# Performance work log

Measured on AMD Instinct MI355X. Metric: run time of the kernel, lower is better.

Reference implementation:

```python
import jax, jax.numpy as jnp
import numpy as np

N = 100000      # nodes
F_IN = 500      # num_features
H = 128         # num_hidden
C = 40          # num_classes
E = 3200000     # structural edges
K = 5           # knn neighbors


def setup_inputs() -> dict:
    key = jax.random.key(0)
    ks = jax.random.split(key, 9)
    x = jax.random.normal(ks[0], (N, F_IN), dtype=jnp.float32)
    edge_index = jax.random.randint(ks[1], (2, E), 0, N, dtype=jnp.int64)
    # knn graph: source i repeated K times, targets random (stand-in for cosine-KNN)
    src = jnp.repeat(jnp.arange(N, dtype=jnp.int64), K)
    dst = jax.random.randint(ks[2], (K * N,), 0, N, dtype=jnp.int64)
    edge_index_knn = jnp.stack([src, dst])
    s = lambda f: np.float32(1.0 / np.sqrt(f))
    W1 = jax.random.normal(ks[3], (F_IN, H), jnp.float32) * s(F_IN)
    b1 = jnp.zeros((H,), jnp.float32)
    W2 = jax.random.normal(ks[4], (2 * H, C), jnp.float32) * s(2 * H)
    b2 = jnp.zeros((C,), jnp.float32)
    Wlin = jax.random.normal(ks[5], (C, 2 * C), jnp.float32) * s(2 * C)  # torch Linear layout [out,in]
    blin = jnp.zeros((C,), jnp.float32)
    return {"x": x, "edge_index": edge_index, "edge_index_knn": edge_index_knn,
            "W1": W1, "b1": b1, "W2": W2, "b2": b2, "Wlin": Wlin, "blin": blin}


def gcn_conv(x, W, b, edge_index):
    # PyG GCNConv: add self-loops, symmetric normalization deg^-1/2 A deg^-1/2, x@W, scatter-add, +bias
    n = x.shape[0]
    loop = jnp.arange(n, dtype=edge_index.dtype)
    row = jnp.concatenate([edge_index[0], loop])  # sources (gathered)
    col = jnp.concatenate([edge_index[1], loop])  # targets (scattered)
    deg = jax.ops.segment_sum(jnp.ones_like(col, x.dtype), col, num_segments=n)
    dinv = jnp.where(deg > 0, jax.lax.rsqrt(jnp.maximum(deg, 1e-12)), 0.0).astype(x.dtype)
    norm = dinv[row] * dinv[col]                      # [E+n]
    h = x @ W                                          # [n, out]
    agg = jax.ops.segment_sum(h[row] * norm[:, None], col, num_segments=n)
    return agg + b


def reference(x, edge_index, edge_index_knn, W1, b1, W2, b2, Wlin, blin):
    h1 = gcn_conv(x, W1, b1, edge_index)
    h1_2 = gcn_conv(x, W1, b1, edge_index_knn)
    R1 = jax.nn.relu(jnp.concatenate([h1, h1_2], axis=1))  # dropout identity (eval mode)
    h2 = gcn_conv(R1, W2, b2, edge_index)
    h2_2 = gcn_conv(R1, W2, b2, edge_index_knn)
    R2 = jnp.concatenate([h2, h2_2], axis=1)
    logits = R2 @ Wlin.T + blin
    return jax.nn.log_softmax(logits, axis=1)
```

## Files before the change

kernel.cpp:

```cpp
#include <hip/hip_runtime.h>
#include <stdint.h>

#define NN   100000
#define FIN  500
#define HID  128
#define KP1  512
#define K2   256
#define CO   40
#define NBUCK 391
#define CAPB_S 9216
#define CAPB_K 1536

typedef __attribute__((ext_vector_type(8))) short short8;
typedef __attribute__((ext_vector_type(4))) float float4v;
typedef __attribute__((address_space(3))) unsigned int as3_u32;
typedef __attribute__((address_space(1))) unsigned int as1_u32;

__device__ __forceinline__ unsigned short f2bf(float f) {
  unsigned u = __float_as_uint(f);
  u = u + 0x7fffu + ((u >> 16) & 1u);
  return (unsigned short)(u >> 16);
}
__device__ __forceinline__ float bf2f(unsigned short s) {
  return __uint_as_float(((unsigned)s) << 16);
}
__device__ __forceinline__ void gl_lds16(const void* g, void* l) {
  __builtin_amdgcn_global_load_lds((const as1_u32*)g, (as3_u32*)l, 16, 0, 0);
}

__global__ __launch_bounds__(256) void k_bin(
    const int* __restrict__ ei, int nS, int nb1S, int* __restrict__ gcur_s, int* __restrict__ gbin_s,
    const int* __restrict__ eik, int nK, int* __restrict__ gcur_k, int* __restrict__ gbin_k) {
  __shared__ int cnt[NBUCK];
  __shared__ int base[NBUCK];
  const int b = blockIdx.x;
  const bool knn = (b >= nb1S);
  const int* src = knn ? eik      : ei;
  const int* tgt = knn ? eik + nK : ei + nS;
  const int n    = knn ? nK : nS;
  int* gcur      = knn ? gcur_k : gcur_s;
  int* gbin      = knn ? gbin_k : gbin_s;
  const int capb = knn ? CAPB_K : CAPB_S;
  const int ebase = (knn ? b - nb1S : b) * 4096;
  const int t = threadIdx.x;

  for (int i = t; i < NBUCK; i += 256) cnt[i] = 0;
  __syncthreads();
  int s[16], g[16];
#pragma unroll
  for (int i = 0; i < 16; ++i) {
    const int e = ebase + i * 256 + t;
    const bool v = e < n;
    s[i] = v ? src[e] : 0;
    g[i] = v ? tgt[e] : -1;
    if (v) atomicAdd(&cnt[g[i] >> 8], 1);
  }
  __syncthreads();
  for (int i = t; i < NBUCK; i += 256) {
    const int c = cnt[i];
    base[i] = c ? atomicAdd(&gcur[i], c) : 0;
    cnt[i] = 0;
  }
  __syncthreads();
#pragma unroll
  for (int i = 0; i < 16; ++i) {
    if (g[i] >= 0) {
      const int bkt = g[i] >> 8;
      const int pos = base[bkt] + atomicAdd(&cnt[bkt], 1);
      if (pos < capb) gbin[bkt * capb + pos] = (s[i] << 8) | (g[i] & 255);
    }
  }
}

__global__ __launch_bounds__(512) void k_bscan(const int* __restrict__ gcur_s, int* __restrict__ bscan_s,
                                               const int* __restrict__ gcur_k, int* __restrict__ bscan_k) {
  __shared__ int sd[512];
  const int* gcur = blockIdx.x ? gcur_k : gcur_s;
  int* bscan      = blockIdx.x ? bscan_k : bscan_s;
  const int t = threadIdx.x;
  const int v = (t < NBUCK) ? gcur[t] : 0;
  sd[t] = v;
  __syncthreads();
  for (int off = 1; off < 512; off <<= 1) {
    const int x = (t >= off) ? sd[t - off] : 0;
    __syncthreads(); sd[t] += x; __syncthreads();
  }
  if (t < NBUCK) bscan[t] = sd[t] - v;
}

__global__ __launch_bounds__(256) void k_csr(
    const int* __restrict__ gcur_s, const int* __restrict__ gbin_s, const int* __restrict__ bscan_s,
    int* __restrict__ rp_s, int* __restrict__ col_s, float* __restrict__ dinv_s,
    const int* __restrict__ gcur_k, const int* __restrict__ gbin_k, const int* __restrict__ bscan_k,
    int* __restrict__ rp_k, int* __restrict__ col_k, float* __restrict__ dinv_k) {
  __shared__ int cnt[256];
  __shared__ int base[256];
  const int b0 = blockIdx.x;
  const bool knn = (b0 >= NBUCK);
  const int b = knn ? b0 - NBUCK : b0;
  const int* gcur  = knn ? gcur_k  : gcur_s;
  const int* gbin  = knn ? gbin_k  : gbin_s;
  const int* bscan = knn ? bscan_k : bscan_s;
  int* rp    = knn ? rp_k   : rp_s;
  int* col   = knn ? col_k  : col_s;
  float* dinv = knn ? dinv_k : dinv_s;
  const int capb = knn ? CAPB_K : CAPB_S;
  const int t = threadIdx.x;
  int nB = gcur[b]; if (nB > capb) nB = capb;
  const int gb0 = b * capb;
  const int gbase = bscan[b];

  cnt[t] = 0;
  __syncthreads();
  for (int i = t; i < nB; i += 256) atomicAdd(&cnt[gbin[gb0 + i] & 255], 1);
  __syncthreads();
  const int myc = cnt[t];
  base[t] = myc;
  __syncthreads();
  for (int off = 1; off < 256; off <<= 1) {
    const int x = (t >= off) ? base[t - off] : 0;
    __syncthreads(); base[t] += x; __syncthreads();
  }
  const int excl = base[t] - myc;
  const int tg = b * 256 + t;
  if (tg < NN) { rp[tg] = gbase + excl; dinv[tg] = rsqrtf((float)(myc + 1)); }
  if (tg == NN) rp[NN] = gbase + excl;
  __syncthreads();
  base[t] = excl; cnt[t] = 0;
  __syncthreads();
  for (int i = t; i < nB; i += 256) {
    const int e = gbin[gb0 + i];
    const int tl = e & 255;
    const int pos = atomicAdd(&cnt[tl], 1);
    col[gbase + base[tl] + pos] = e >> 8;
  }
}

__global__ void k_w1t(const float* __restrict__ W1, unsigned short* __restrict__ W1T) {
  int idx = blockIdx.x * 256 + threadIdx.x;
  int n = idx >> 9, k = idx & 511;
  float v = (k < FIN) ? W1[k * HID + n] : 0.f;
  W1T[idx] = f2bf(v);
}
__global__ void k_w2t(const float* __restrict__ W2, unsigned short* __restrict__ W2T) {
  int idx = blockIdx.x * 256 + threadIdx.x;
  int n = idx >> 8, k = idx & 255;
  float v = (n < CO) ? W2[k * CO + n] : 0.f;
  W2T[idx] = f2bf(v);
}

__global__ __launch_bounds__(256) void k_gemm1(const float* __restrict__ x,
    const unsigned short* __restrict__ W1T, const float* __restrict__ zbuf,
    unsigned short* __restrict__ H1b) {
  __shared__ float Als[1024 * 4];
  __shared__ unsigned short Bls[512 * 8];
  const int t = threadIdx.x;
  const int wv = t >> 6, lane = t & 63;
  const int qd = lane >> 4, mr = lane & 15;
  const int m0 = blockIdx.x * 128;

  float4v acc[2][8];
  const float4v zf4 = {0.f, 0.f, 0.f, 0.f};
#pragma unroll
  for (int a = 0; a < 2; ++a)
#pragma unroll
    for (int b = 0; b < 8; ++b) acc[a][b] = zf4;

  for (int kk = 0; kk < 16; ++kk) {
    const int k0 = kk * 32;
    __syncthreads();
#pragma unroll
    for (int i = 0; i < 4; ++i) {
      const int cb = (wv * 4 + i) * 64;
      const int q = cb + lane;
      const int kg = q >> 7, m = q & 127;
      const int gm = m0 + m, kb = k0 + kg * 4;
      const float* gp = (gm < NN && kb < FIN) ? (x + (size_t)gm * FIN + kb) : zbuf;
      gl_lds16(gp, &Als[cb * 4]);
    }
#pragma unroll
    for (int i = 0; i < 2; ++i) {
      const int cb = (wv * 2 + i) * 64;
      const int q = cb + lane;
      const int kg = q >> 7, n = q & 127;
      const unsigned short* gp = W1T + n * KP1 + k0 + kg * 8;
      gl_lds16(gp, &Bls[cb * 8]);
    }
    __syncthreads();
    short8 af[2];
#pragma unroll
    for (int rt = 0; rt < 2; ++rt) {
      const int m = wv * 32 + rt * 16 + mr;
      const float4v a0 = *(const float4v*)&Als[((2 * qd) * 128 + m) * 4];
      const float4v a1 = *(const float4v*)&Als[((2 * qd + 1) * 128 + m) * 4];
      short8 f;
      f[0] = (short)f2bf(a0[0]); f[1] = (short)f2bf(a0[1]);
      f[2] = (short)f2bf(a0[2]); f[3] = (short)f2bf(a0[3]);
      f[4] = (short)f2bf(a1[0]); f[5] = (short)f2bf(a1[1]);
      f[6] = (short)f2bf(a1[2]); f[7] = (short)f2bf(a1[3]);
      af[rt] = f;
    }
#pragma unroll
    for (int ct = 0; ct < 8; ++ct) {
      const short8 bf = *(const short8*)&Bls[(qd * 128 + ct * 16 + mr) * 8];
      acc[0][ct] = __builtin_amdgcn_mfma_f32_16x16x32_bf16(af[0], bf, acc[0][ct], 0, 0, 0);
      acc[1][ct] = __builtin_amdgcn_mfma_f32_16x16x32_bf16(af[1], bf, acc[1][ct], 0, 0, 0);
    }
  }
#pragma unroll
  for (int rt = 0; rt < 2; ++rt) {
    const int rb = m0 + wv * 32 + rt * 16 + qd * 4;
#pragma unroll
    for (int ct = 0; ct < 8; ++ct) {
      const int col = ct * 16 + mr;
#pragma unroll
      for (int j = 0; j < 4; ++j) {
        const int r = rb + j;
        if (r < NN) H1b[(size_t)r * HID + col] = f2bf(acc[rt][ct][j]);
      }
    }
  }
}

__global__ __launch_bounds__(256) void k_gemm2(const unsigned short* __restrict__ R1b,
    const unsigned short* __restrict__ W2T, const unsigned short* __restrict__ zbuf,
    unsigned short* __restrict__ H2b) {
  __shared__ unsigned short Als[512 * 8];
  __shared__ unsigned short Bls[192 * 8];
  const int t = threadIdx.x;
  const int wv = t >> 6, lane = t & 63;
  const int qd = lane >> 4, mr = lane & 15;
  const int m0 = blockIdx.x * 128;

  float4v acc[2][3];
  const float4v zf4 = {0.f, 0.f, 0.f, 0.f};
#pragma unroll
  for (int a = 0; a < 2; ++a)
#pragma unroll
    for (int b = 0; b < 3; ++b) acc[a][b] = zf4;

  for (int kk = 0; kk < 8; ++kk) {
    const int k0 = kk * 32;
    __syncthreads();
#pragma unroll
    for (int i = 0; i < 2; ++i) {
      const int cb = (wv * 2 + i) * 64;
      const int q = cb + lane;
      const int kg = q >> 7, m = q & 127;
      const int gm = m0 + m;
      const unsigned short* gp = (gm < NN) ? (R1b + (size_t)gm * K2 + k0 + kg * 8) : zbuf;
      gl_lds16(gp, &Als[cb * 8]);
    }
    if (wv < 3) {
      const int cb = wv * 64;
      const int q = cb + lane;
      const int kg = q / 48, n = q % 48;
      const unsigned short* gp = W2T + n * K2 + k0 + kg * 8;
      gl_lds16(gp, &Bls[cb * 8]);
    }
    __syncthreads();
    short8 af[2];
#pragma unroll
    for (int rt = 0; rt < 2; ++rt)
      af[rt] = *(const short8*)&Als[(qd * 128 + wv * 32 + rt * 16 + mr) * 8];
#pragma unroll
    for (int ct = 0; ct < 3; ++ct) {
      const short8 bf = *(const short8*)&Bls[(qd * 48 + ct * 16 + mr) * 8];
      acc[0][ct] = __builtin_amdgcn_mfma_f32_16x16x32_bf16(af[0], bf, acc[0][ct], 0, 0, 0);
      acc[1][ct] = __builtin_amdgcn_mfma_f32_16x16x32_bf16(af[1], bf, acc[1][ct], 0, 0, 0);
    }
  }
#pragma unroll
  for (int rt = 0; rt < 2; ++rt) {
    const int rb = m0 + wv * 32 + rt * 16 + qd * 4;
#pragma unroll
    for (int ct = 0; ct < 3; ++ct) {
      const int col = ct * 16 + mr;
      if (col < CO) {
#pragma unroll
        for (int j = 0; j < 4; ++j) {
          const int r = rb + j;
          if (r < NN) H2b[(size_t)r * CO + col] = f2bf(acc[rt][ct][j]);
        }
      }
    }
  }
}

__global__ __launch_bounds__(256) void k_agg1(
    const int* __restrict__ rp_s, const int* __restrict__ col_s, const float* __restrict__ dinv_s,
    const int* __restrict__ rp_k, const int* __restrict__ col_k, const float* __restrict__ dinv_k,
    const unsigned short* __restrict__ H, const float* __restrict__ bias,
    unsigned short* __restrict__ out, int nbS) {
  const int b = blockIdx.x;
  const bool knn = (b >= nbS);
  const int* rp = knn ? rp_k : rp_s;
  const int* ci = knn ? col_k : col_s;
  const float* dinv = knn ? dinv_k : dinv_s;
  const int colOff = knn ? HID : 0;
  const int wv = threadIdx.x >> 6, lane = threadIdx.x & 63;
  const int c = (knn ? b - nbS : b) * 4 + wv;
  if (c >= NN) return;
  const float dc = dinv[c];
  const unsigned pc = ((const unsigned*)(H + (size_t)c * HID))[lane];
  float ax = dc * bf2f((unsigned short)(pc & 0xffffu));
  float ay = dc * bf2f((unsigned short)(pc >> 16));
  int e = rp[c];
  const int e1 = rp[c + 1];
  for (; e + 4 <= e1; e += 4) {
    const int r0 = ci[e], r1 = ci[e + 1], r2 = ci[e + 2], r3 = ci[e + 3];
    const float d0 = dinv[r0], d1 = dinv[r1], d2 = dinv[r2], d3 = dinv[r3];
    const unsigned p0 = ((const unsigned*)(H + (size_t)r0 * HID))[lane];
    const unsigned p1 = ((const unsigned*)(H + (size_t)r1 * HID))[lane];
    const unsigned p2 = ((const unsigned*)(H + (size_t)r2 * HID))[lane];
    const unsigned p3 = ((const unsigned*)(H + (size_t)r3 * HID))[lane];
    ax += d0 * bf2f((unsigned short)(p0 & 0xffffu)) + d1 * bf2f((unsigned short)(p1 & 0xffffu))
        + d2 * bf2f((unsigned short)(p2 & 0xffffu)) + d3 * bf2f((unsigned short)(p3 & 0xffffu));
    ay += d0 * bf2f((unsigned short)(p0 >> 16)) + d1 * bf2f((unsigned short)(p1 >> 16))
        + d2 * bf2f((unsigned short)(p2 >> 16)) + d3 * bf2f((unsigned short)(p3 >> 16));
  }
  for (; e < e1; ++e) {
    const int r = ci[e];
    const float d = dinv[r];
    const unsigned pr = ((const unsigned*)(H + (size_t)r * HID))[lane];
    ax += d * bf2f((unsigned short)(pr & 0xffffu));
    ay += d * bf2f((unsigned short)(pr >> 16));
  }
  const float2 bb = ((const float2*)bias)[lane];
  const float o0 = fmaxf(dc * ax + bb.x, 0.f);
  const float o1 = fmaxf(dc * ay + bb.y, 0.f);
  const unsigned pk = (unsigned)f2bf(o0) | ((unsigned)f2bf(o1) << 16);
  ((unsigned*)(out + (size_t)c * (2 * HID) + colOff))[lane] = pk;
}

__global__ __launch_bounds__(256) void k_agg2(
    const int* __restrict__ rp_s, const int* __restrict__ col_s, const float* __restrict__ dinv_s,
    const int* __restrict__ rp_k, const int* __restrict__ col_k, const float* __restrict__ dinv_k,
    const unsigned short* __restrict__ H2, const float* __restrict__ bias,
    unsigned short* __restrict__ R2, int nbS) {
  const int b = blockIdx.x;
  const bool knn = (b >= nbS);
  const int* rp = knn ? rp_k : rp_s;
  const int* ci = knn ? col_k : col_s;
  const float* dinv = knn ? dinv_k : dinv_s;
  const int colOff = knn ? CO : 0;
  const int wv = threadIdx.x >> 6, lane = threadIdx.x & 63;
  const int c = (knn ? b - nbS : b) * 4 + wv;
  if (c >= NN || lane >= CO) return;
  const float dc = dinv[c];
  float acc = dc * bf2f(H2[(size_t)c * CO + lane]);
  int e = rp[c];
  const int e1 = rp[c + 1];
  for (; e + 4 <= e1; e += 4) {
    const int r0 = ci[e], r1 = ci[e + 1], r2 = ci[e + 2], r3 = ci[e + 3];
    const float d0 = dinv[r0], d1 = dinv[r1], d2 = dinv[r2], d3 = dinv[r3];
    acc += d0 * bf2f(H2[(size_t)r0 * CO + lane]) + d1 * bf2f(H2[(size_t)r1 * CO + lane])
         + d2 * bf2f(H2[(size_t)r2 * CO + lane]) + d3 * bf2f(H2[(size_t)r3 * CO + lane]);
  }
  for (; e < e1; ++e) {
    const int r = ci[e];
    acc += dinv[r] * bf2f(H2[(size_t)r * CO + lane]);
  }
  R2[(size_t)c * 80 + colOff + lane] = f2bf(dc * acc + bias[lane]);
}

__global__ __launch_bounds__(256) void k_final(const unsigned short* __restrict__ R2,
    const float* __restrict__ Wlin, const float* __restrict__ blin,
    float* __restrict__ out) {
  __shared__ float rw[32 * 81];
  __shared__ float wl[40 * 81];
  __shared__ float bl[40];
  const int t = threadIdx.x;
  const int n0 = blockIdx.x * 32;
  for (int i = t; i < 2560; i += 256) rw[(i / 80) * 81 + (i % 80)] = bf2f(R2[(size_t)n0 * 80 + i]);
  for (int i = t; i < 3200; i += 256) wl[(i / 80) * 81 + (i % 80)] = Wlin[i];
  if (t < 40) bl[t] = blin[t];
  __syncthreads();
  const int nl = t >> 3, jg = t & 7;
  const int j0 = jg * 5;
  float lg[5];
#pragma unroll
  for (int jj = 0; jj < 5; ++jj) lg[jj] = bl[j0 + jj];
#pragma unroll 4
  for (int k = 0; k < 80; ++k) {
    const float v = rw[nl * 81 + k];
#pragma unroll
    for (int jj = 0; jj < 5; ++jj) lg[jj] += v * wl[(j0 + jj) * 81 + k];
  }
  float mx = lg[0];
#pragma unroll
  for (int jj = 1; jj < 5; ++jj) mx = fmaxf(mx, lg[jj]);
  mx = fmaxf(mx, __shfl_xor(mx, 1));
  mx = fmaxf(mx, __shfl_xor(mx, 2));
  mx = fmaxf(mx, __shfl_xor(mx, 4));
  float s = 0.f;
#pragma unroll
  for (int jj = 0; jj < 5; ++jj) s += expf(lg[jj] - mx);
  s += __shfl_xor(s, 1);
  s += __shfl_xor(s, 2);
  s += __shfl_xor(s, 4);
  const float lse = mx + logf(s);
  const int n = n0 + nl;
#pragma unroll
  for (int jj = 0; jj < 5; ++jj) out[(size_t)n * CO + j0 + jj] = lg[jj] - lse;
}

extern "C" void kernel_launch(void* const* d_in, const int* in_sizes, int n_in,
                              void* d_out, int out_size, void* d_ws, size_t ws_size,
                              hipStream_t stream) {
  const float* x  = (const float*)d_in[0];
  const int* ei   = (const int*)d_in[1];
  const int* eik  = (const int*)d_in[2];
  const float* W1 = (const float*)d_in[3];
  const float* b1 = (const float*)d_in[4];
  const float* W2 = (const float*)d_in[5];
  const float* b2 = (const float*)d_in[6];
  const float* Wl = (const float*)d_in[7];
  const float* bl = (const float*)d_in[8];
  float* out = (float*)d_out;
  const int E  = in_sizes[1] / 2;
  const int EK = in_sizes[2] / 2;

  char* p = (char*)d_ws;
  size_t off = 0;
  auto alloc = [&](size_t bytes) -> void* {
    void* r = (void*)(p + off);
    off += (bytes + 255) & ~(size_t)255;
    return r;
  };
  int* gcur_s = (int*)alloc((size_t)NBUCK * 4);
  int* gcur_k = (int*)alloc((size_t)NBUCK * 4);
  void* zbuf = alloc(256);
  const size_t zero_span = off;
  int* bscan_s = (int*)alloc((size_t)NBUCK * 4);
  int* bscan_k = (int*)alloc((size_t)NBUCK * 4);
  float* dinv_s = (float*)alloc((size_t)NN * 4);
  float* dinv_k = (float*)alloc((size_t)NN * 4);
  int* rp_s = (int*)alloc((size_t)(NN + 1) * 4);
  int* rp_k = (int*)alloc((size_t)(NN + 1) * 4);
  unsigned short* W1T = (unsigned short*)alloc((size_t)HID * KP1 * 2);
  unsigned short* W2T = (unsigned short*)alloc((size_t)48 * K2 * 2);
  int* gbin_s = (int*)alloc((size_t)NBUCK * CAPB_S * 4);
  int* gbin_k = (int*)alloc((size_t)NBUCK * CAPB_K * 4);
  int* col_s = (int*)alloc((size_t)E * 4);
  int* col_k = (int*)alloc((size_t)EK * 4);
  unsigned short* H1b = (unsigned short*)alloc((size_t)NN * HID * 2);
  unsigned short* R1b = (unsigned short*)alloc((size_t)NN * K2 * 2);
  unsigned short* H2b = (unsigned short*)alloc((size_t)NN * CO * 2);
  unsigned short* R2  = H1b;

  hipMemsetAsync(d_ws, 0, zero_span, stream);

  const int nb1S = (E + 4095) / 4096;
  const int nb1K = (EK + 4095) / 4096;
  k_bin<<<nb1S + nb1K, 256, 0, stream>>>(ei, E, nb1S, gcur_s, gbin_s, eik, EK, gcur_k, gbin_k);
  k_bscan<<<2, 512, 0, stream>>>(gcur_s, bscan_s, gcur_k, bscan_k);
  k_csr<<<2 * NBUCK, 256, 0, stream>>>(gcur_s, gbin_s, bscan_s, rp_s, col_s, dinv_s,
                                       gcur_k, gbin_k, bscan_k, rp_k, col_k, dinv_k);

  k_w1t<<<(HID * KP1) / 256, 256, 0, stream>>>(W1, W1T);
  k_w2t<<<(48 * K2) / 256, 256, 0, stream>>>(W2, W2T);

  k_gemm1<<<(NN + 127) / 128, 256, 0, stream>>>(x, W1T, (const float*)zbuf, H1b);
  const int nbAgg = (NN + 3) / 4;
  k_agg1<<<2 * nbAgg, 256, 0, stream>>>(rp_s, col_s, dinv_s, rp_k, col_k, dinv_k,
                                        H1b, b1, R1b, nbAgg);

  k_gemm2<<<(NN + 127) / 128, 256, 0, stream>>>(R1b, W2T, (const unsigned short*)zbuf, H2b);
  k_agg2<<<2 * nbAgg, 256, 0, stream>>>(rp_s, col_s, dinv_s, rp_k, col_k, dinv_k,
                                        H2b, b2, R2, nbAgg);

  k_final<<<NN / 32, 256, 0, stream>>>(R2, Wl, bl, out);
}
```

Baseline: 793.8 us.

## Fold final linear into layer-2 weights, fuse aggregation with log-softmax, prebake edge weights

Layer 2 and the final linear are folded algebraically: W2 is premultiplied with the two halves of Wlin into an 80-column weight, and the biases into one constant vector. The second aggregation then reads the 80-wide P/Q product and applies log-softmax directly, which removes the H2/R2 round trips and the separate final kernel. A new pass stores each edge's source dinv next to its column index in an int2 CSR, so aggregation no longer does a dependent dinv gather. Layer-1 aggregation now handles both graphs per node in one wave and prefetches edges in batches of eight. The cost is doubled CSR index bytes, an extra fuse pass over all edges, and a change in where bf16 rounding happens.

```diff
diff --git a/kernel.cpp b/kernel.cpp
--- a/kernel.cpp
+++ b/kernel.cpp
@@ -7,6 +7,7 @@
 #define KP1  512
 #define K2   256
 #define CO   40
+#define NPQ  80
 #define NBUCK 391
 #define CAPB_S 9216
 #define CAPB_K 1536
@@ -90,9 +91,9 @@
 
 __global__ __launch_bounds__(256) void k_csr(
     const int* __restrict__ gcur_s, const int* __restrict__ gbin_s, const int* __restrict__ bscan_s,
-    int* __restrict__ rp_s, int* __restrict__ col_s, float* __restrict__ dinv_s,
+    int* __restrict__ rp_s, int2* __restrict__ colw_s, float* __restrict__ dinv_s,
     const int* __restrict__ gcur_k, const int* __restrict__ gbin_k, const int* __restrict__ bscan_k,
-    int* __restrict__ rp_k, int* __restrict__ col_k, float* __restrict__ dinv_k) {
+    int* __restrict__ rp_k, int2* __restrict__ colw_k, float* __restrict__ dinv_k) {
   __shared__ int cnt[256];
   __shared__ int base[256];
   const int b0 = blockIdx.x;
@@ -101,8 +102,8 @@
   const int* gcur  = knn ? gcur_k  : gcur_s;
   const int* gbin  = knn ? gbin_k  : gbin_s;
   const int* bscan = knn ? bscan_k : bscan_s;
-  int* rp    = knn ? rp_k   : rp_s;
-  int* col   = knn ? col_k  : col_s;
+  int* rp     = knn ? rp_k   : rp_s;
+  int2* colw  = knn ? colw_k : colw_s;
   float* dinv = knn ? dinv_k : dinv_s;
   const int capb = knn ? CAPB_K : CAPB_S;
   const int t = threadIdx.x;
@@ -132,7 +133,26 @@
     const int e = gbin[gb0 + i];
     const int tl = e & 255;
     const int pos = atomicAdd(&cnt[tl], 1);
-    col[gbase + base[tl] + pos] = e >> 8;
+    colw[gbase + base[tl] + pos] = make_int2(e >> 8, 0);
+  }
+}
+
+__global__ __launch_bounds__(256) void k_fuse(
+    int2* __restrict__ colw_s, const float* __restrict__ dinv_s, int nS, int nbF,
+    int2* __restrict__ colw_k, const float* __restrict__ dinv_k, int nK) {
+  const int b = blockIdx.x;
+  if (b < nbF) {
+    const int i = b * 256 + threadIdx.x;
+    if (i < nS) {
+      const int s = colw_s[i].x;
+      colw_s[i].y = __float_as_int(dinv_s[s]);
+    }
+  } else {
+    const int i = (b - nbF) * 256 + threadIdx.x;
+    if (i < nK) {
+      const int s = colw_k[i].x;
+      colw_k[i].y = __float_as_int(dinv_k[s]);
+    }
   }
 }
 
@@ -142,11 +162,23 @@
   float v = (k < FIN) ? W1[k * HID + n] : 0.f;
   W1T[idx] = f2bf(v);
 }
-__global__ void k_w2t(const float* __restrict__ W2, unsigned short* __restrict__ W2T) {
-  int idx = blockIdx.x * 256 + threadIdx.x;
-  int n = idx >> 8, k = idx & 255;
-  float v = (n < CO) ? W2[k * CO + n] : 0.f;
-  W2T[idx] = f2bf(v);
+__global__ void k_wpq(const float* __restrict__ W2, const float* __restrict__ Wl,
+                      const float* __restrict__ b2, const float* __restrict__ bl,
+                      unsigned short* __restrict__ WpqT, float* __restrict__ cb) {
+  const int idx = blockIdx.x * 256 + threadIdx.x;
+  const int n = idx >> 8, k = idx & 255;
+  const int o = (n < CO) ? n : n - CO;
+  const int joff = (n < CO) ? 0 : CO;
+  float s = 0.f;
+#pragma unroll 8
+  for (int j = 0; j < CO; ++j) s += W2[k * CO + j] * Wl[o * NPQ + joff + j];
+  WpqT[n * K2 + k] = f2bf(s);
+  if (blockIdx.x == 0 && threadIdx.x < CO) {
+    const int oo = threadIdx.x;
+    float c = bl[oo];
+    for (int j = 0; j < CO; ++j) c += b2[j] * (Wl[oo * NPQ + j] + Wl[oo * NPQ + CO + j]);
+    cb[oo] = c;
+  }
 }
 
 __global__ __launch_bounds__(256) void k_gemm1(const float* __restrict__ x,
@@ -223,21 +255,21 @@
 }
 
 __global__ __launch_bounds__(256) void k_gemm2(const unsigned short* __restrict__ R1b,
-    const unsigned short* __restrict__ W2T, const unsigned short* __restrict__ zbuf,
-    unsigned short* __restrict__ H2b) {
+    const unsigned short* __restrict__ WpqT, const unsigned short* __restrict__ zbuf,
+    unsigned short* __restrict__ PQ) {
   __shared__ unsigned short Als[512 * 8];
-  __shared__ unsigned short Bls[192 * 8];
+  __shared__ unsigned short Bls[320 * 8];
   const int t = threadIdx.x;
   const int wv = t >> 6, lane = t & 63;
   const int qd = lane >> 4, mr = lane & 15;
   const int m0 = blockIdx.x * 128;
 
-  float4v acc[2][3];
+  float4v acc[2][5];
   const float4v zf4 = {0.f, 0.f, 0.f, 0.f};
 #pragma unroll
   for (int a = 0; a < 2; ++a)
 #pragma unroll
-    for (int b = 0; b < 3; ++b) acc[a][b] = zf4;
+    for (int b = 0; b < 5; ++b) acc[a][b] = zf4;
 
   for (int kk = 0; kk < 8; ++kk) {
     const int k0 = kk * 32;
@@ -251,12 +283,17 @@
       const unsigned short* gp = (gm < NN) ? (R1b + (size_t)gm * K2 + k0 + kg * 8) : zbuf;
       gl_lds16(gp, &Als[cb * 8]);
     }
-    if (wv < 3) {
+    {
       const int cb = wv * 64;
       const int q = cb + lane;
-      const int kg = q / 48, n = q % 48;
-      const unsigned short* gp = W2T + n * K2 + k0 + kg * 8;
-      gl_lds16(gp, &Bls[cb * 8]);
+      const int kg = q / 80, n = q % 80;
+      gl_lds16(WpqT + n * K2 + k0 + kg * 8, &Bls[cb * 8]);
+      if (wv == 0) {
+        const int cb2 = 4 * 64;
+        const int q2 = cb2 + lane;
+        const int kg2 = q2 / 80, n2 = q2 % 80;
+        gl_lds16(WpqT + n2 * K2 + k0 + kg2 * 8, &Bls[cb2 * 8]);
+      }
     }
     __syncthreads();
     short8 af[2];
@@ -264,8 +301,8 @@
     for (int rt = 0; rt < 2; ++rt)
       af[rt] = *(const short8*)&Als[(qd * 128 + wv * 32 + rt * 16 + mr) * 8];
 #pragma unroll
-    for (int ct = 0; ct < 3; ++ct) {
-      const short8 bf = *(const short8*)&Bls[(qd * 48 + ct * 16 + mr) * 8];
+    for (int ct = 0; ct < 5; ++ct) {
+      const short8 bf = *(const short8*)&Bls[(qd * 80 + ct * 16 + mr) * 8];
       acc[0][ct] = __builtin_amdgcn_mfma_f32_16x16x32_bf16(af[0], bf, acc[0][ct], 0, 0, 0);
       acc[1][ct] = __builtin_amdgcn_mfma_f32_16x16x32_bf16(af[1], bf, acc[1][ct], 0, 0, 0);
     }
@@ -274,135 +311,159 @@
   for (int rt = 0; rt < 2; ++rt) {
     const int rb = m0 + wv * 32 + rt * 16 + qd * 4;
 #pragma unroll
-    for (int ct = 0; ct < 3; ++ct) {
+    for (int ct = 0; ct < 5; ++ct) {
       const int col = ct * 16 + mr;
-      if (col < CO) {
-#pragma unroll
-        for (int j = 0; j < 4; ++j) {
-          const int r = rb + j;
-          if (r < NN) H2b[(size_t)r * CO + col] = f2bf(acc[rt][ct][j]);
-        }
-      }
-    }
+#pragma unroll
+      for (int j = 0; j < 4; ++j) {
+        const int r = rb + j;
+        if (r < NN) PQ[(size_t)r * NPQ + col] = f2bf(acc[rt][ct][j]);
+      }
+    }
+  }
+}
+
+__device__ __forceinline__ void agg_row128(const int2* __restrict__ cw, int e0, int e1,
+    const unsigned* __restrict__ H32, int lane, float& ax, float& ay) {
+  const int nb = (e1 - e0) & ~7;
+  int e = e0;
+  if (nb) {
+    int2 q[8];
+#pragma unroll
+    for (int j = 0; j < 8; ++j) q[j] = cw[e + j];
+    for (int base = 0; base < nb; base += 8) {
+      int2 qn[8];
+      const bool more = (base + 8 < nb);
+      if (more) {
+#pragma unroll
+        for (int j = 0; j < 8; ++j) qn[j] = cw[e + base + 8 + j];
+      }
+#pragma unroll
+      for (int j = 0; j < 8; ++j) {
+        const unsigned d = H32[(size_t)q[j].x * 64 + lane];
+        const float w = __int_as_float(q[j].y);
+        ax += w * __uint_as_float(d << 16);
+        ay += w * __uint_as_float(d & 0xffff0000u);
+      }
+      if (more) {
+#pragma unroll
+        for (int j = 0; j < 8; ++j) q[j] = qn[j];
+      }
+    }
+    e += nb;
+  }
+  for (; e < e1; ++e) {
+    const int2 q = cw[e];
+    const unsigned d = H32[(size_t)q.x * 64 + lane];
+    const float w = __int_as_float(q.y);
+    ax += w * __uint_as_float(d << 16);
+    ay += w * __uint_as_float(d & 0xffff0000u);
   }
 }
 
 __global__ __launch_bounds__(256) void k_agg1(
-    const int* __restrict__ rp_s, const int* __restrict__ col_s, const float* __restrict__ dinv_s,
-    const int* __restrict__ rp_k, const int* __restrict__ col_k, const float* __restrict__ dinv_k,
+    const int* __restrict__ rp_s, const int2* __restrict__ colw_s, const float* __restrict__ dinv_s,
+    const int* __restrict__ rp_k, const int2* __restrict__ colw_k, const float* __restrict__ dinv_k,
     const unsigned short* __restrict__ H, const float* __restrict__ bias,
-    unsigned short* __restrict__ out, int nbS) {
-  const int b = blockIdx.x;
-  const bool knn = (b >= nbS);
-  const int* rp = knn ? rp_k : rp_s;
-  const int* ci = knn ? col_k : col_s;
-  const float* dinv = knn ? dinv_k : dinv_s;
-  const int colOff = knn ? HID : 0;
+    unsigned short* __restrict__ out) {
   const int wv = threadIdx.x >> 6, lane = threadIdx.x & 63;
-  const int c = (knn ? b - nbS : b) * 4 + wv;
+  const int c = blockIdx.x * 4 + wv;
   if (c >= NN) return;
-  const float dc = dinv[c];
-  const unsigned pc = ((const unsigned*)(H + (size_t)c * HID))[lane];
-  float ax = dc * bf2f((unsigned short)(pc & 0xffffu));
-  float ay = dc * bf2f((unsigned short)(pc >> 16));
-  int e = rp[c];
-  const int e1 = rp[c + 1];
-  for (; e + 4 <= e1; e += 4) {
-    const int r0 = ci[e], r1 = ci[e + 1], r2 = ci[e + 2], r3 = ci[e + 3];
-    const float d0 = dinv[r0], d1 = dinv[r1], d2 = dinv[r2], d3 = dinv[r3];
-    const unsigned p0 = ((const unsigned*)(H + (size_t)r0 * HID))[lane];
-    const unsigned p1 = ((const unsigned*)(H + (size_t)r1 * HID))[lane];
-    const unsigned p2 = ((const unsigned*)(H + (size_t)r2 * HID))[lane];
-    const unsigned p3 = ((const unsigned*)(H + (size_t)r3 * HID))[lane];
-    ax += d0 * bf2f((unsigned short)(p0 & 0xffffu)) + d1 * bf2f((unsigned short)(p1 & 0xffffu))
-        + d2 * bf2f((unsigned short)(p2 & 0xffffu)) + d3 * bf2f((unsigned short)(p3 & 0xffffu));
-    ay += d0 * bf2f((unsigned short)(p0 >> 16)) + d1 * bf2f((unsigned short)(p1 >> 16))
-        + d2 * bf2f((unsigned short)(p2 >> 16)) + d3 * bf2f((unsigned short)(p3 >> 16));
-  }
-  for (; e < e1; ++e) {
-    const int r = ci[e];
-    const float d = dinv[r];
-    const unsigned pr = ((const unsigned*)(H + (size_t)r * HID))[lane];
-    ax += d * bf2f((unsigned short)(pr & 0xffffu));
-    ay += d * bf2f((unsigned short)(pr >> 16));
-  }
+  const unsigned* H32 = (const unsigned*)H;
+  const float dcs = dinv_s[c];
+  const float dck = dinv_k[c];
+  const unsigned pc = H32[(size_t)c * 64 + lane];
+  const float slo = __uint_as_float(pc << 16);
+  const float shi = __uint_as_float(pc & 0xffff0000u);
+  float ax = dcs * slo, ay = dcs * shi;
+  float bx = dck * slo, by = dck * shi;
+  agg_row128(colw_s, rp_s[c], rp_s[c + 1], H32, lane, ax, ay);
+  agg_row128(colw_k, rp_k[c], rp_k[c + 1], H32, lane, bx, by);
   const float2 bb = ((const float2*)bias)[lane];
-  const float o0 = fmaxf(dc * ax + bb.x, 0.f);
-  const float o1 = fmaxf(dc * ay + bb.y, 0.f);
-  const unsigned pk = (unsigned)f2bf(o0) | ((unsigned)f2bf(o1) << 16);
-  ((unsigned*)(out + (size_t)c * (2 * HID) + colOff))[lane] = pk;
-}
-
-__global__ __launch_bounds__(256) void k_agg2(
-    const int* __restrict__ rp_s, const int* __restrict__ col_s, const float* __restrict__ dinv_s,
-    const int* __restrict__ rp_k, const int* __restrict__ col_k, const float* __restrict__ dinv_k,
-    const unsigned short* __restrict__ H2, const float* __restrict__ bias,
-    unsigned short* __restrict__ R2, int nbS) {
-  const int b = blockIdx.x;
-  const bool knn = (b >= nbS);
-  const int* rp = knn ? rp_k : rp_s;
-  const int* ci = knn ? col_k : col_s;
-  const float* dinv = knn ? dinv_k : dinv_s;
-  const int colOff = knn ? CO : 0;
+  const float o0 = fmaxf(dcs * ax + bb.x, 0.f);
+  const float o1 = fmaxf(dcs * ay + bb.y, 0.f);
+  const float o2 = fmaxf(dck * bx + bb.x, 0.f);
+  const float o3 = fmaxf(dck * by + bb.y, 0.f);
+  unsigned* orow = (unsigned*)(out + (size_t)c * K2);
+  orow[lane]      = (unsigned)f2bf(o0) | ((unsigned)f2bf(o1) << 16);
+  orow[64 + lane] = (unsigned)f2bf(o2) | ((unsigned)f2bf(o3) << 16);
+}
+
+__global__ __launch_bounds__(256) void k_aggf(
+    const int* __restrict__ rp_s, const int2* __restrict__ colw_s, const float* __restrict__ dinv_s,
+    const int* __restrict__ rp_k, const int2* __restrict__ colw_k, const float* __restrict__ dinv_k,
+    const unsigned short* __restrict__ PQ, const float* __restrict__ cb,
+    float* __restrict__ out) {
   const int wv = threadIdx.x >> 6, lane = threadIdx.x & 63;
-  const int c = (knn ? b - nbS : b) * 4 + wv;
-  if (c >= NN || lane >= CO) return;
-  const float dc = dinv[c];
-  float acc = dc * bf2f(H2[(size_t)c * CO + lane]);
-  int e = rp[c];
-  const int e1 = rp[c + 1];
-  for (; e + 4 <= e1; e += 4) {
-    const int r0 = ci[e], r1 = ci[e + 1], r2 = ci[e + 2], r3 = ci[e + 3];
-    const float d0 = dinv[r0], d1 = dinv[r1], d2 = dinv[r2], d3 = dinv[r3];
-    acc += d0 * bf2f(H2[(size_t)r0 * CO + lane]) + d1 * bf2f(H2[(size_t)r1 * CO + lane])
-         + d2 * bf2f(H2[(size_t)r2 * CO + lane]) + d3 * bf2f(H2[(size_t)r3 * CO + lane]);
-  }
-  for (; e < e1; ++e) {
-    const int r = ci[e];
-    acc += dinv[r] * bf2f(H2[(size_t)r * CO + lane]);
-  }
-  R2[(size_t)c * 80 + colOff + lane] = f2bf(dc * acc + bias[lane]);
-}
-
-__global__ __launch_bounds__(256) void k_final(const unsigned short* __restrict__ R2,
-    const float* __restrict__ Wlin, const float* __restrict__ blin,
-    float* __restrict__ out) {
-  __shared__ float rw[32 * 81];
-  __shared__ float wl[40 * 81];
-  __shared__ float bl[40];
-  const int t = threadIdx.x;
-  const int n0 = blockIdx.x * 32;
-  for (int i = t; i < 2560; i += 256) rw[(i / 80) * 81 + (i % 80)] = bf2f(R2[(size_t)n0 * 80 + i]);
-  for (int i = t; i < 3200; i += 256) wl[(i / 80) * 81 + (i % 80)] = Wlin[i];
-  if (t < 40) bl[t] = blin[t];
-  __syncthreads();
-  const int nl = t >> 3, jg = t & 7;
-  const int j0 = jg * 5;
-  float lg[5];
-#pragma unroll
-  for (int jj = 0; jj < 5; ++jj) lg[jj] = bl[j0 + jj];
-#pragma unroll 4
-  for (int k = 0; k < 80; ++k) {
-    const float v = rw[nl * 81 + k];
-#pragma unroll
-    for (int jj = 0; jj < 5; ++jj) lg[jj] += v * wl[(j0 + jj) * 81 + k];
-  }
-  float mx = lg[0];
-#pragma unroll
-  for (int jj = 1; jj < 5; ++jj) mx = fmaxf(mx, lg[jj]);
-  mx = fmaxf(mx, __shfl_xor(mx, 1));
-  mx = fmaxf(mx, __shfl_xor(mx, 2));
-  mx = fmaxf(mx, __shfl_xor(mx, 4));
-  float s = 0.f;
-#pragma unroll
-  for (int jj = 0; jj < 5; ++jj) s += expf(lg[jj] - mx);
-  s += __shfl_xor(s, 1);
-  s += __shfl_xor(s, 2);
-  s += __shfl_xor(s, 4);
-  const float lse = mx + logf(s);
-  const int n = n0 + nl;
-#pragma unroll
-  for (int jj = 0; jj < 5; ++jj) out[(size_t)n * CO + j0 + jj] = lg[jj] - lse;
+  const int c = blockIdx.x * 4 + wv;
+  if (c >= NN) return;
+  const unsigned* PQ32 = (const unsigned*)PQ;
+  const int g = lane / 20;
+  const int l = lane % 20;
+  float sx = 0.f, sy = 0.f, kx = 0.f, ky = 0.f;
+  if (g < 3) {
+    {
+      const int e1 = rp_s[c + 1];
+      int e = rp_s[c] + g;
+      for (; e + 9 < e1; e += 12) {
+        const int2 q0 = colw_s[e], q1 = colw_s[e + 3], q2 = colw_s[e + 6], q3 = colw_s[e + 9];
+        const unsigned d0 = PQ32[(size_t)q0.x * 40 + l];
+        const unsigned d1 = PQ32[(size_t)q1.x * 40 + l];
+        const unsigned d2 = PQ32[(size_t)q2.x * 40 + l];
+        const unsigned d3 = PQ32[(size_t)q3.x * 40 + l];
+        const float w0 = __int_as_float(q0.y), w1 = __int_as_float(q1.y);
+        const float w2 = __int_as_float(q2.y), w3 = __int_as_float(q3.y);
+        sx += w0 * __uint_as_float(d0 << 16) + w1 * __uint_as_float(d1 << 16)
+            + w2 * __uint_as_float(d2 << 16) + w3 * __uint_as_float(d3 << 16);
+        sy += w0 * __uint_as_float(d0 & 0xffff0000u) + w1 * __uint_as_float(d1 & 0xffff0000u)
+            + w2 * __uint_as_float(d2 & 0xffff0000u) + w3 * __uint_as_float(d3 & 0xffff0000u);
+      }
+      for (; e < e1; e += 3) {
+        const int2 q = colw_s[e];
+        const unsigned d = PQ32[(size_t)q.x * 40 + l];
+        const float w = __int_as_float(q.y);
+        sx += w * __uint_as_float(d << 16);
+        sy += w * __uint_as_float(d & 0xffff0000u);
+      }
+    }
+    {
+      const int e1 = rp_k[c + 1];
+      int e = rp_k[c] + g;
+      for (; e < e1; e += 3) {
+        const int2 q = colw_k[e];
+        const unsigned d = PQ32[(size_t)q.x * 40 + 20 + l];
+        const float w = __int_as_float(q.y);
+        kx += w * __uint_as_float(d << 16);
+        ky += w * __uint_as_float(d & 0xffff0000u);
+      }
+    }
+  }
+  sx += __shfl(sx, lane + 20) + __shfl(sx, lane + 40);
+  sy += __shfl(sy, lane + 20) + __shfl(sy, lane + 40);
+  kx += __shfl(kx, lane + 20) + __shfl(kx, lane + 40);
+  ky += __shfl(ky, lane + 20) + __shfl(ky, lane + 40);
+
+  float lo = 0.f, hi = 0.f;
+  if (lane < 20) {
+    const float dcs = dinv_s[c], dck = dinv_k[c];
+    const unsigned dP = PQ32[(size_t)c * 40 + lane];
+    const unsigned dQ = PQ32[(size_t)c * 40 + 20 + lane];
+    const float2 cbb = ((const float2*)cb)[lane];
+    lo = dcs * (sx + dcs * __uint_as_float(dP << 16))
+       + dck * (kx + dck * __uint_as_float(dQ << 16)) + cbb.x;
+    hi = dcs * (sy + dcs * __uint_as_float(dP & 0xffff0000u))
+       + dck * (ky + dck * __uint_as_float(dQ & 0xffff0000u)) + cbb.y;
+  }
+  float m = (lane < 20) ? fmaxf(lo, hi) : -3.4e38f;
+#pragma unroll
+  for (int off = 1; off < 64; off <<= 1) m = fmaxf(m, __shfl_xor(m, off));
+  float s = (lane < 20) ? (expf(lo - m) + expf(hi - m)) : 0.f;
+#pragma unroll
+  for (int off = 1; off < 64; off <<= 1) s += __shfl_xor(s, off);
+  const float lse = m + logf(s);
+  if (lane < 20) {
+    float2 o; o.x = lo - lse; o.y = hi - lse;
+    ((float2*)(out + (size_t)c * CO))[lane] = o;
+  }
 }
 
 extern "C" void kernel_launch(void* const* d_in, const int* in_sizes, int n_in,
@@ -439,15 +500,15 @@
   int* rp_s = (int*)alloc((size_t)(NN + 1) * 4);
   int* rp_k = (int*)alloc((size_t)(NN + 1) * 4);
   unsigned short* W1T = (unsigned short*)alloc((size_t)HID * KP1 * 2);
-  unsigned short* W2T = (unsigned short*)alloc((size_t)48 * K2 * 2);
+  unsigned short* WpqT = (unsigned short*)alloc((size_t)NPQ * K2 * 2);
+  float* cbv = (float*)alloc((size_t)CO * 4);
   int* gbin_s = (int*)alloc((size_t)NBUCK * CAPB_S * 4);
   int* gbin_k = (int*)alloc((size_t)NBUCK * CAPB_K * 4);
-  int* col_s = (int*)alloc((size_t)E * 4);
-  int* col_k = (int*)alloc((size_t)EK * 4);
+  int2* colw_s = (int2*)alloc((size_t)E * 8);
+  int2* colw_k = (int2*)alloc((size_t)EK * 8);
   unsigned short* H1b = (unsigned short*)alloc((size_t)NN * HID * 2);
   unsigned short* R1b = (unsigned short*)alloc((size_t)NN * K2 * 2);
-  unsigned short* H2b = (unsigned short*)alloc((size_t)NN * CO * 2);
-  unsigned short* R2  = H1b;
+  unsigned short* PQ = H1b;
 
   hipMemsetAsync(d_ws, 0, zero_span, stream);
 
@@ -455,20 +516,19 @@
   const int nb1K = (EK + 4095) / 4096;
   k_bin<<<nb1S + nb1K, 256, 0, stream>>>(ei, E, nb1S, gcur_s, gbin_s, eik, EK, gcur_k, gbin_k);
   k_bscan<<<2, 512, 0, stream>>>(gcur_s, bscan_s, gcur_k, bscan_k);
-  k_csr<<<2 * NBUCK, 256, 0, stream>>>(gcur_s, gbin_s, bscan_s, rp_s, col_s, dinv_s,
-                                       gcur_k, gbin_k, bscan_k, rp_k, col_k, dinv_k);
+  k_csr<<<2 * NBUCK, 256, 0, stream>>>(gcur_s, gbin_s, bscan_s, rp_s, colw_s, dinv_s,
+                                       gcur_k, gbin_k, bscan_k, rp_k, colw_k, dinv_k);
+  const int nbF = (E + 255) / 256;
+  const int nbFk = (EK + 255) / 256;
+  k_fuse<<<nbF + nbFk, 256, 0, stream>>>(colw_s, dinv_s, E, nbF, colw_k, dinv_k, EK);
 
   k_w1t<<<(HID * KP1) / 256, 256, 0, stream>>>(W1, W1T);
-  k_w2t<<<(48 * K2) / 256, 256, 0, stream>>>(W2, W2T);
+  k_wpq<<<NPQ, 256, 0, stream>>>(W2, Wl, b2, bl, WpqT, cbv);
 
   k_gemm1<<<(NN + 127) / 128, 256, 0, stream>>>(x, W1T, (const float*)zbuf, H1b);
   const int nbAgg = (NN + 3) / 4;
-  k_agg1<<<2 * nbAgg, 256, 0, stream>>>(rp_s, col_s, dinv_s, rp_k, col_k, dinv_k,
-                                        H1b, b1, R1b, nbAgg);
-
-  k_gemm2<<<(NN + 127) / 128, 256, 0, stream>>>(R1b, W2T, (const unsigned short*)zbuf, H2b);
-  k_agg2<<<2 * nbAgg, 256, 0, stream>>>(rp_s, col_s, dinv_s, rp_k, col_k, dinv_k,
-                                        H2b, b2, R2, nbAgg);
-
-  k_final<<<NN / 32, 256, 0, stream>>>(R2, Wl, bl, out);
-}
+  k_agg1<<<nbAgg, 256, 0, stream>>>(rp_s, colw_s, dinv_s, rp_k, colw_k, dinv_k, H1b, b1, R1b);
+
+  k_gemm2<<<(NN + 127) / 128, 256, 0, stream>>>(R1b, WpqT, (const unsigned short*)zbuf, PQ);
+  k_aggf<<<nbAgg, 256, 0, stream>>>(rp_s, colw_s, dinv_s, rp_k, colw_k, dinv_k, PQ, cbv, out);
+}
```

After: 761.2 us. -4.1%, faster.
